# Performance work log

Measured on AMD Instinct MI355X. Metric: run time of the kernel, lower is better.

Reference implementation:

```python
import jax, jax.numpy as jnp
import numpy as np

KEY_DIM = 64
SCALE_PER_SEQ = 1.0 / np.sqrt(KEY_DIM).astype(np.float32)
SCALE_OVER_SEQS = 1.0 / np.sqrt(KEY_DIM).astype(np.float32)


def setup_inputs() -> dict:
    key = jax.random.key(0)
    ks = jax.random.split(key, 6)
    b, i, t, j, d, dv, kd = 4, 512, 32, 256, 512, 512, KEY_DIM
    w_scale = 0.05
    return {
        "input_seq": jax.random.normal(ks[0], (b, i, d), jnp.float32),
        "memory_x": jax.random.normal(ks[1], (b, t, j, d), jnp.float32),
        "memory_y": jax.random.normal(ks[2], (b, t, j, dv), jnp.float32),
        "Wq": jax.random.normal(ks[3], (d, kd), jnp.float32) * w_scale,
        "bq": jnp.zeros((kd,), jnp.float32),
        "Wk": jax.random.normal(ks[4], (d, kd), jnp.float32) * w_scale,
        "bk": jnp.zeros((kd,), jnp.float32),
        "Wv": jax.random.normal(ks[5], (dv, dv), jnp.float32) * w_scale,
        "bv": jnp.zeros((dv,), jnp.float32),
    }


def reference(input_seq, memory_x, memory_y, Wq, bq, Wk, bk, Wv, bv):
    # Projections (Dense layers)
    queries = input_seq @ Wq + bq          # [b, i, kd]
    keys = memory_x @ Wk + bk              # [b, t, j, kd]
    values = memory_y @ Wv + bv            # [b, t, j, dv]

    # Level 1: within-sequence attention
    attn_mat = jnp.einsum('bik,btjk->btij', queries, keys)          # [b, t, i, j]
    per_seq_attn = jax.nn.softmax(SCALE_PER_SEQ * attn_mat, axis=-1)
    per_seq_retrieved = jnp.einsum('btij,btjk->btik', per_seq_attn, values)  # [b, t, i, dv]

    # Level 2: over-sequences attention (max-reduce over j, softmax over t)
    mem_seq_attn = jnp.max(attn_mat, axis=-1)                       # [b, t, i]
    mem_seq_attn = jax.nn.softmax(SCALE_OVER_SEQS * mem_seq_attn, axis=1)

    retrieved = jnp.einsum('bti,btik->bik', mem_seq_attn, per_seq_retrieved)  # [b, i, dv]
    return retrieved
```

## Files before the change

### kernel.cpp

```cpp
#include <hip/hip_runtime.h>
#include <cstdint>

#define B_ 4
#define I_ 512
#define T_ 32
#define J_ 256
#define D_ 512
#define DV_ 512
#define KD_ 64
#define TJ_ (T_*J_)
#define BI_ (B_*I_)
#define MK_ (B_*T_*J_)

typedef unsigned short u16;
typedef __attribute__((ext_vector_type(8))) u16 u16x8;
typedef __attribute__((ext_vector_type(4))) u16 u16x4;
typedef __attribute__((ext_vector_type(8))) short bf16x8;
typedef __attribute__((ext_vector_type(4))) float f32x4;

__device__ __forceinline__ u16 f2bf(float f){
  unsigned u = __float_as_uint(f);
  u += 0x7fffu + ((u >> 16) & 1u);
  return (u16)(u >> 16);
}
__device__ __forceinline__ float bf2f(u16 h){ return __uint_as_float(((unsigned)h) << 16); }

#define GLD16(gsrc, ldst) __builtin_amdgcn_global_load_lds( \
    (const __attribute__((address_space(1))) unsigned int*)(gsrc), \
    (__attribute__((address_space(3))) unsigned int*)(ldst), 16, 0, 0)

__global__ __launch_bounds__(256) void k_prep(const float* __restrict__ Y, u16* __restrict__ Yt,
                                              const float* __restrict__ Wq, const float* __restrict__ Wk,
                                              const float* __restrict__ Wv, u16* __restrict__ wqt,
                                              u16* __restrict__ wkt, u16* __restrict__ wvt){
  __shared__ __align__(16) u16 tileT[64][72];
  int bid = blockIdx.x;
  int tid = threadIdx.x;
  if (bid < 4096){
    int kx = bid & 127, ny = (bid >> 7) & 7, b = bid >> 10;
    int k0 = kx*64, n0 = ny*64;
    #pragma unroll
    for (int s=0;s<4;++s){
      int idx = tid + s*256; int r = idx>>4, c4 = idx&15;
      const float4 v = *(const float4*)&Y[((size_t)b*TJ_ + k0 + r)*DV_ + n0 + c4*4];
      tileT[c4*4+0][r] = f2bf(v.x);
      tileT[c4*4+1][r] = f2bf(v.y);
      tileT[c4*4+2][r] = f2bf(v.z);
      tileT[c4*4+3][r] = f2bf(v.w);
    }
    __syncthreads();
    #pragma unroll
    for (int s=0;s<2;++s){
      int idx = tid + s*256; int rn = idx>>3, c8 = idx&7;
      *(u16x8*)&Yt[((size_t)b*DV_ + n0 + rn)*TJ_ + k0 + c8*8] = *(const u16x8*)&tileT[rn][c8*8];
    }
  } else {
    int gid = (bid - 4096)*256 + tid;
    if (gid < 32768){
      int n = gid >> 9, k = gid & 511;
      wqt[gid] = f2bf(Wq[(size_t)k*64 + n]);
    } else if (gid < 65536){
      int g = gid - 32768;
      int n = g >> 9, k = g & 511;
      wkt[g] = f2bf(Wk[(size_t)k*64 + n]);
    } else {
      int g = gid - 65536;
      int n = g >> 9, k = g & 511;
      wvt[g] = f2bf(Wv[(size_t)k*512 + n]);
    }
  }
}

__global__ __launch_bounds__(256) void k_proj(const float* __restrict__ mx, const float* __restrict__ iseq,
                                              const u16* __restrict__ wkt, const u16* __restrict__ wqt,
                                              const float* __restrict__ bk, const float* __restrict__ bq,
                                              u16* __restrict__ kbf, u16* __restrict__ qbf){
  __shared__ __align__(16) u16 As[32][72];
  __shared__ __align__(16) u16 Bs[64][72];
  int bid = blockIdx.x;
  const float* A; const u16* Bt; const float* bias; u16* C; int row0;
  if (bid < 1024){ A = mx;   Bt = wkt; bias = bk; C = kbf; row0 = bid*32; }
  else           { A = iseq; Bt = wqt; bias = bq; C = qbf; row0 = (bid-1024)*32; }
  int tid = threadIdx.x;
  int lane = tid & 63, wv = tid >> 6;
  int lrow = lane & 15, lk8 = (lane >> 4) * 8;
  int mf = wv >> 1, nfb = (wv & 1) * 2;
  int ar = tid >> 4, ac4 = tid & 15;
  int br = tid >> 3, bc8 = tid & 7;
  f32x4 acc[2];
  acc[0] = (f32x4){0.f,0.f,0.f,0.f}; acc[1] = (f32x4){0.f,0.f,0.f,0.f};

  float4 fa[2][2]; u16x8 fb[2][2];
  #define PROJ_LOAD(pp, k0) { \
    fa[pp][0] = *(const float4*)&A[(size_t)(row0 + ar)*512 + (k0) + ac4*4]; \
    fa[pp][1] = *(const float4*)&A[(size_t)(row0 + ar + 16)*512 + (k0) + ac4*4]; \
    fb[pp][0] = *(const u16x8*)&Bt[(size_t)br*512 + (k0) + bc8*8]; \
    fb[pp][1] = *(const u16x8*)&Bt[(size_t)(br+32)*512 + (k0) + bc8*8]; }

  PROJ_LOAD(0, 0)
  #pragma unroll
  for (int t=0;t<8;++t){
    const int p = t & 1;
    if (t) __syncthreads();
    if (t < 7) PROJ_LOAD(p^1, (t+1)*64)
    #pragma unroll
    for (int s=0;s<2;++s){
      u16x4 o; o[0]=f2bf(fa[p][s].x); o[1]=f2bf(fa[p][s].y); o[2]=f2bf(fa[p][s].z); o[3]=f2bf(fa[p][s].w);
      *(u16x4*)&As[ar + 16*s][ac4*4] = o;
      *(u16x8*)&Bs[br + 32*s][bc8*8] = fb[p][s];
    }
    __syncthreads();
    #pragma unroll
    for (int kk=0;kk<2;++kk){
      bf16x8 a = *(const bf16x8*)&As[mf*16 + lrow][kk*32 + lk8];
      #pragma unroll
      for (int n2=0;n2<2;++n2){
        bf16x8 bb = *(const bf16x8*)&Bs[(nfb+n2)*16 + lrow][kk*32 + lk8];
        acc[n2] = __builtin_amdgcn_mfma_f32_16x16x32_bf16(a, bb, acc[n2], 0, 0, 0);
      }
    }
  }
  #undef PROJ_LOAD
  __syncthreads();
  u16* R = &As[0][0];
  #pragma unroll
  for (int n2=0;n2<2;++n2)
    #pragma unroll
    for (int r=0;r<4;++r){
      int row = mf*16 + (lane>>4)*4 + r;
      int col = (nfb+n2)*16 + lrow;
      R[row*64 + col] = f2bf(acc[n2][r] + bias[col]);
    }
  __syncthreads();
  {
    int row = tid >> 3, c8 = tid & 7;
    *(u16x8*)&C[(size_t)(row0+row)*64 + c8*8] = *(const u16x8*)&R[row*64 + c8*8];
  }
}

__global__ __launch_bounds__(256) void k_score(const u16* __restrict__ Qbf, const u16* __restrict__ Kbf,
                                               u16* __restrict__ P, float* __restrict__ mb, float* __restrict__ zb){
  __shared__ __align__(16) u16 Qs[64][72];
  __shared__ __align__(16) u16 Ks[256][72];
  __shared__ float smax[4][64];
  __shared__ float ssum[4][64];
  __shared__ float mrow[64];
  int tid = threadIdx.x;
  int i0 = blockIdx.x*64, t = blockIdx.y, b = blockIdx.z;
  int lane = tid & 63, wv = tid >> 6;
  int lrow = lane & 15, lk = (lane >> 4) * 8;

  #pragma unroll
  for (int s=0;s<2;++s){
    int idx = tid + s*256; int r = idx>>3, c8 = idx&7;
    *(u16x8*)&Qs[r][c8*8] = *(const u16x8*)&Qbf[((size_t)b*I_ + i0 + r)*KD_ + c8*8];
  }
  #pragma unroll
  for (int s=0;s<8;++s){
    int idx = tid + s*256; int r = idx>>3, c8 = idx&7;
    *(u16x8*)&Ks[r][c8*8] = *(const u16x8*)&Kbf[(((size_t)b*T_ + t)*J_ + r)*KD_ + c8*8];
  }
  __syncthreads();

  f32x4 acc[4][4];
  #pragma unroll
  for (int i=0;i<4;++i)
    #pragma unroll
    for (int j=0;j<4;++j) acc[i][j] = (f32x4){0.f,0.f,0.f,0.f};

  #pragma unroll
  for (int kk=0;kk<2;++kk){
    bf16x8 a[4], bb[4];
    #pragma unroll
    for (int mf=0;mf<4;++mf) a[mf] = *(const bf16x8*)&Qs[mf*16 + lrow][kk*32 + lk];
    #pragma unroll
    for (int nf=0;nf<4;++nf) bb[nf] = *(const bf16x8*)&Ks[wv*64 + nf*16 + lrow][kk*32 + lk];
    #pragma unroll
    for (int mf=0;mf<4;++mf)
      #pragma unroll
      for (int nf=0;nf<4;++nf)
        acc[mf][nf] = __builtin_amdgcn_mfma_f32_16x16x32_bf16(a[mf], bb[nf], acc[mf][nf], 0, 0, 0);
  }

  #pragma unroll
  for (int mf=0;mf<4;++mf)
    #pragma unroll
    for (int r=0;r<4;++r){
      float v = acc[mf][0][r];
      #pragma unroll
      for (int nf=1;nf<4;++nf) v = fmaxf(v, acc[mf][nf][r]);
      v = fmaxf(v, __shfl_xor(v, 1));
      v = fmaxf(v, __shfl_xor(v, 2));
      v = fmaxf(v, __shfl_xor(v, 4));
      v = fmaxf(v, __shfl_xor(v, 8));
      if (lrow == 0) smax[wv][mf*16 + (lane>>4)*4 + r] = v;
    }
  __syncthreads();
  if (tid < 64){
    float m = fmaxf(fmaxf(smax[0][tid], smax[1][tid]), fmaxf(smax[2][tid], smax[3][tid]));
    mrow[tid] = m;
    mb[((size_t)b*T_ + t)*I_ + i0 + tid] = m;
  }
  __syncthreads();

  #pragma unroll
  for (int mf=0;mf<4;++mf)
    #pragma unroll
    for (int r=0;r<4;++r){
      int row = mf*16 + (lane>>4)*4 + r;
      float M = mrow[row];
      float ssm = 0.f;
      #pragma unroll
      for (int nf=0;nf<4;++nf){
        float p = __expf(0.125f*(acc[mf][nf][r] - M));
        acc[mf][nf][r] = p;
        ssm += p;
      }
      ssm += __shfl_xor(ssm, 1);
      ssm += __shfl_xor(ssm, 2);
      ssm += __shfl_xor(ssm, 4);
      ssm += __shfl_xor(ssm, 8);
      if (lrow == 0) ssum[wv][row] = ssm;
    }
  __syncthreads();
  if (tid < 64){
    float z = ssum[0][tid] + ssum[1][tid] + ssum[2][tid] + ssum[3][tid];
    zb[((size_t)b*T_ + t)*I_ + i0 + tid] = z;
  }

  u16* Ps = &Ks[0][0];
  #pragma unroll
  for (int mf=0;mf<4;++mf)
    #pragma unroll
    for (int nf=0;nf<4;++nf)
      #pragma unroll
      for (int r=0;r<4;++r){
        int row = mf*16 + (lane>>4)*4 + r;
        int col = wv*64 + nf*16 + lrow;
        Ps[row*264 + col] = f2bf(acc[mf][nf][r]);
      }
  __syncthreads();
  #pragma unroll
  for (int s=0;s<8;++s){
    int idx = tid + s*256; int r = idx>>5, c8 = idx&31;
    *(u16x8*)&P[(((size_t)b*T_ + t)*I_ + i0 + r)*J_ + c8*8] = *(const u16x8*)&Ps[r*264 + c8*8];
  }
}

template<int CH>
__global__ __launch_bounds__(256,4) void k_passB(const u16* __restrict__ P, const float* __restrict__ mbp,
                                                 const float* __restrict__ zbp, const u16* __restrict__ Yt,
                                                 u16* __restrict__ Up){
  constexpr int TPC = T_/CH;
  constexpr int NS = TPC*4;
  __shared__ __align__(16) u16 As[128*64];
  __shared__ __align__(16) u16 Bs[64*64];
  __shared__ float cs[TPC][128];
  int tid = threadIdx.x;
  int lane = tid & 63, wv = tid >> 6, wm = wv >> 1, wn = wv & 1;
  int lrow = lane & 15, lg = lane >> 4;

  int logical = (blockIdx.x & 7)*128 + (blockIdx.x >> 3);
  int group = logical >> 5, within = logical & 31;
  int ix = within & 3, ny = within >> 2;
  int b = group / CH, ch = group % CH;
  int i0 = ix*128, n0 = ny*64;

  int l8 = lane >> 3, sl = lane & 7;

  auto STAGE = [&](int step){
    int tt = step >> 2, st = step & 3;
    int t = ch*TPC + tt, j0 = st*64;
    const u16* Pbase = &P[(((size_t)b*T_ + t)*I_ + i0)*J_];
    const u16* Ybase = &Yt[((size_t)b*DV_ + n0)*TJ_ + (size_t)t*J_];
    #pragma unroll
    for (int s=0;s<4;++s){
      int row = (wv*4+s)*8 + l8;
      int colA = j0 + ((sl ^ (row & 7)) << 3);
      GLD16(Pbase + (size_t)row*J_ + colA, (u16*)As + (wv*4+s)*512);
    }
    #pragma unroll
    for (int s=0;s<2;++s){
      int row = (wv*2+s)*8 + l8;
      int colA = j0 + ((sl ^ (row & 7)) << 3);
      GLD16(Ybase + (size_t)row*TJ_ + colA, (u16*)Bs + (wv*2+s)*512);
    }
  };

  STAGE(0);

  if (tid < 128){
    int i = i0 + tid;
    float w[T_];
    float lmax = -3.0e38f;
    #pragma unroll
    for (int t=0;t<T_;++t){
      float mt = 0.125f * mbp[((size_t)b*T_ + t)*I_ + i];
      w[t] = mt;
      lmax = fmaxf(lmax, mt);
    }
    float W = 0.f;
    #pragma unroll
    for (int t=0;t<T_;++t){ float e = __expf(w[t] - lmax); w[t] = e; W += e; }
    float inv = 1.f / W;
    #pragma unroll
    for (int tt=0;tt<TPC;++tt)
      cs[tt][tid] = w[ch*TPC+tt] * inv / zbp[((size_t)b*T_ + ch*TPC + tt)*I_ + i];
  }
  __syncthreads();

  f32x4 acc[4][2];
  #pragma unroll
  for (int i=0;i<4;++i)
    #pragma unroll
    for (int j=0;j<2;++j) acc[i][j] = (f32x4){0.f,0.f,0.f,0.f};

  for (int tt = 0; tt < TPC; ++tt){
    if (tt){
      #pragma unroll
      for (int mf=0;mf<4;++mf)
        #pragma unroll
        for (int r=0;r<4;++r){
          int row = wm*64 + mf*16 + lg*4 + r;
          float ratio = cs[tt-1][row] / cs[tt][row];
          #pragma unroll
          for (int nf=0;nf<2;++nf) acc[mf][nf][r] *= ratio;
        }
    }
    #pragma unroll
    for (int st = 0; st < 4; ++st){
      const int step = tt*4 + st;
      #pragma unroll
      for (int kk=0;kk<2;++kk){
        bf16x8 a[4], bb[2];
        #pragma unroll
        for (int mf=0;mf<4;++mf){
          int ar = wm*64 + mf*16 + lrow;
          int off = ar*128 + ((kk*64 + lg*16) ^ ((ar & 7) << 4));
          a[mf] = *(const bf16x8*)((const char*)As + off);
        }
        #pragma unroll
        for (int nf=0;nf<2;++nf){
          int br = wn*32 + nf*16 + lrow;
          int off = br*128 + ((kk*64 + lg*16) ^ ((br & 7) << 4));
          bb[nf] = *(const bf16x8*)((const char*)Bs + off);
        }
        #pragma unroll
        for (int mf=0;mf<4;++mf)
          #pragma unroll
          for (int nf=0;nf<2;++nf)
            acc[mf][nf] = __builtin_amdgcn_mfma_f32_16x16x32_bf16(a[mf], bb[nf], acc[mf][nf], 0, 0, 0);
      }
      if (step + 1 < NS){
        __syncthreads();
        STAGE(step + 1);
        __syncthreads();
      }
    }
  }

  __syncthreads();
  u16* R = (u16*)&As[0];
  #pragma unroll
  for (int mf=0;mf<4;++mf)
    #pragma unroll
    for (int r=0;r<4;++r){
      int row = wm*64 + mf*16 + lg*4 + r;
      float cfin = cs[TPC-1][row];
      #pragma unroll
      for (int nf=0;nf<2;++nf){
        int col = wn*32 + nf*16 + lrow;
        R[row*64 + col] = f2bf(acc[mf][nf][r] * cfin);
      }
    }
  __syncthreads();
  u16* Ub = &Up[(size_t)ch*BI_*DV_ + ((size_t)b*I_ + i0)*DV_ + n0];
  #pragma unroll
  for (int s=0;s<4;++s){
    int id = tid + s*256;
    int row = id >> 3, c8 = id & 7;
    *(u16x8*)&Ub[(size_t)row*DV_ + c8*8] = *(const u16x8*)&R[row*64 + c8*8];
  }
}

template<int CH>
__global__ __launch_bounds__(256) void k_final(const u16* __restrict__ Up, const u16* __restrict__ Bt,
                                               const float* __restrict__ bv, float* __restrict__ out){
  __shared__ __align__(16) u16 As[32][72];
  __shared__ __align__(16) u16 Bs[64][72];
  int tid = threadIdx.x;
  int lane = tid & 63, wv = tid >> 6;
  int lrow = lane & 15, lk8 = (lane >> 4) * 8;
  int bid = blockIdx.x;
  int swz = (bid & 7)*64 + (bid >> 3);
  int row0 = (swz >> 3)*32, col0 = (swz & 7)*64;
  int mf = wv >> 1, nfb = (wv & 1)*2;
  const size_t S = (size_t)BI_*DV_;
  int ar = tid >> 3, ac8 = tid & 7;
  f32x4 acc[2];
  acc[0] = (f32x4){0.f,0.f,0.f,0.f}; acc[1] = (f32x4){0.f,0.f,0.f,0.f};

  u16x8 pa[2][CH]; u16x8 rb[2][2];
  #define FIN_LOAD(pp, k0) { \
    _Pragma("unroll") \
    for (int c=0;c<CH;++c) pa[pp][c] = *(const u16x8*)&Up[(size_t)c*S + (size_t)(row0+ar)*512 + (k0) + ac8*8]; \
    _Pragma("unroll") \
    for (int s=0;s<2;++s) rb[pp][s] = *(const u16x8*)&Bt[(size_t)(col0 + (tid>>3) + 32*s)*512 + (k0) + ac8*8]; }

  FIN_LOAD(0, 0)
  #pragma unroll
  for (int t=0;t<8;++t){
    const int p = t & 1;
    if (t) __syncthreads();
    if (t < 7) FIN_LOAD(p^1, (t+1)*64)
    u16x8 o;
    #pragma unroll
    for (int e=0;e<8;++e){
      float v = 0.f;
      #pragma unroll
      for (int c=0;c<CH;++c) v += bf2f(pa[p][c][e]);
      o[e] = f2bf(v);
    }
    *(u16x8*)&As[ar][ac8*8] = o;
    #pragma unroll
    for (int s=0;s<2;++s) *(u16x8*)&Bs[(tid>>3) + 32*s][ac8*8] = rb[p][s];
    __syncthreads();
    #pragma unroll
    for (int kk=0;kk<2;++kk){
      bf16x8 a = *(const bf16x8*)&As[mf*16 + lrow][kk*32 + lk8];
      #pragma unroll
      for (int n2=0;n2<2;++n2){
        bf16x8 bb = *(const bf16x8*)&Bs[(nfb+n2)*16 + lrow][kk*32 + lk8];
        acc[n2] = __builtin_amdgcn_mfma_f32_16x16x32_bf16(a, bb, acc[n2], 0, 0, 0);
      }
    }
  }
  #undef FIN_LOAD
  #pragma unroll
  for (int n2=0;n2<2;++n2)
    #pragma unroll
    for (int r=0;r<4;++r){
      int row = row0 + mf*16 + (lane>>4)*4 + r;
      int col = col0 + (nfb+n2)*16 + lrow;
      out[(size_t)row*DV_ + col] = acc[n2][r] + bv[col];
    }
}

extern "C" void kernel_launch(void* const* d_in, const int* in_sizes, int n_in,
                              void* d_out, int out_size, void* d_ws, size_t ws_size,
                              hipStream_t stream){
  const float* input_seq = (const float*)d_in[0];
  const float* memory_x  = (const float*)d_in[1];
  const float* memory_y  = (const float*)d_in[2];
  const float* Wq = (const float*)d_in[3];
  const float* bq = (const float*)d_in[4];
  const float* Wk = (const float*)d_in[5];
  const float* bk = (const float*)d_in[6];
  const float* Wv = (const float*)d_in[7];
  const float* bv = (const float*)d_in[8];
  float* out = (float*)d_out;

  char* ws = (char*)d_ws;
  size_t off = 0;
  auto alloc = [&](size_t bytes)->void*{
    void* p = ws + off; off += (bytes + 255) & ~(size_t)255; return p;
  };
  u16*   wqt = (u16*)  alloc((size_t)KD_*D_*2);
  u16*   wkt = (u16*)  alloc((size_t)KD_*D_*2);
  u16*   wvt = (u16*)  alloc((size_t)DV_*DV_*2);
  u16*   qbf = (u16*)  alloc((size_t)BI_*KD_*2);
  u16*   kbf = (u16*)  alloc((size_t)MK_*KD_*2);
  u16*   yt  = (u16*)  alloc((size_t)B_*DV_*TJ_*2);
  u16*   Pb  = (u16*)  alloc((size_t)B_*T_*I_*J_*2);
  float* mb  = (float*)alloc((size_t)B_*T_*I_*4);
  float* zb  = (float*)alloc((size_t)B_*T_*I_*4);
  u16*   Up  = (u16*)  alloc((size_t)8*BI_*DV_*2);

  k_prep<<<4096 + 1280, 256, 0, stream>>>(memory_y, yt, Wq, Wk, Wv, wqt, wkt, wvt);
  k_proj<<<1024 + 64, 256, 0, stream>>>(memory_x, input_seq, wkt, wqt, bk, bq, kbf, qbf);
  k_score<<<dim3(I_/64, T_, B_), 256, 0, stream>>>(qbf, kbf, Pb, mb, zb);
  k_passB<8><<<32*B_*8, 256, 0, stream>>>(Pb, mb, zb, yt, Up);
  k_final<8><<<512, 256, 0, stream>>>(Up, wvt, bv, out);
}
```

Before: 96.19 us.

## Load P operand directly to registers and double-buffer value tiles in LDS

In the pass-B GEMM, the P operand is now read straight from global memory into registers instead of being staged through LDS. The value-operand (Yt) tile is double-buffered in LDS, with the next tile's load issued before the current step's MFMAs. This drops from two barriers per k-step to one, and shrinks LDS use. The cost is that each A element is now fetched from global memory by both column waves, and those per-lane 16-byte loads are strided by a full row, so they coalesce less well than the old staged path.

```diff
diff --git a/kernel.cpp b/kernel.cpp
--- a/kernel.cpp
+++ b/kernel.cpp
@@ -253,8 +253,7 @@
                                                  u16* __restrict__ Up){
   constexpr int TPC = T_/CH;
   constexpr int NS = TPC*4;
-  __shared__ __align__(16) u16 As[128*64];
-  __shared__ __align__(16) u16 Bs[64*64];
+  __shared__ __align__(16) u16 Bs[2][64*64];
   __shared__ float cs[TPC][128];
   int tid = threadIdx.x;
   int lane = tid & 63, wv = tid >> 6, wm = wv >> 1, wn = wv & 1;
@@ -268,26 +267,19 @@
 
   int l8 = lane >> 3, sl = lane & 7;
 
-  auto STAGE = [&](int step){
+  auto STAGEB = [&](int step, int pp){
     int tt = step >> 2, st = step & 3;
     int t = ch*TPC + tt, j0 = st*64;
-    const u16* Pbase = &P[(((size_t)b*T_ + t)*I_ + i0)*J_];
     const u16* Ybase = &Yt[((size_t)b*DV_ + n0)*TJ_ + (size_t)t*J_];
-    #pragma unroll
-    for (int s=0;s<4;++s){
-      int row = (wv*4+s)*8 + l8;
-      int colA = j0 + ((sl ^ (row & 7)) << 3);
-      GLD16(Pbase + (size_t)row*J_ + colA, (u16*)As + (wv*4+s)*512);
-    }
     #pragma unroll
     for (int s=0;s<2;++s){
       int row = (wv*2+s)*8 + l8;
       int colA = j0 + ((sl ^ (row & 7)) << 3);
-      GLD16(Ybase + (size_t)row*TJ_ + colA, (u16*)Bs + (wv*2+s)*512);
+      GLD16(Ybase + (size_t)row*TJ_ + colA, (u16*)Bs[pp] + (wv*2+s)*512);
     }
   };
 
-  STAGE(0);
+  STAGEB(0, 0);
 
   if (tid < 128){
     int i = i0 + tid;
@@ -327,40 +319,40 @@
           for (int nf=0;nf<2;++nf) acc[mf][nf][r] *= ratio;
         }
     }
+    int t = ch*TPC + tt;
+    const u16* Pbase = &P[(((size_t)b*T_ + t)*I_ + i0)*J_];
     #pragma unroll
     for (int st = 0; st < 4; ++st){
       const int step = tt*4 + st;
+      const int pp = step & 1;
+      const u16* Pj = Pbase + st*64;
+      bf16x8 a[2][4];
+      #pragma unroll
+      for (int kk=0;kk<2;++kk)
+        #pragma unroll
+        for (int mf=0;mf<4;++mf)
+          a[kk][mf] = *(const bf16x8*)&Pj[(size_t)(wm*64 + mf*16 + lrow)*J_ + kk*32 + lg*8];
+      if (step + 1 < NS) STAGEB(step+1, pp^1);
       #pragma unroll
       for (int kk=0;kk<2;++kk){
-        bf16x8 a[4], bb[2];
-        #pragma unroll
-        for (int mf=0;mf<4;++mf){
-          int ar = wm*64 + mf*16 + lrow;
-          int off = ar*128 + ((kk*64 + lg*16) ^ ((ar & 7) << 4));
-          a[mf] = *(const bf16x8*)((const char*)As + off);
-        }
+        bf16x8 bb[2];
         #pragma unroll
         for (int nf=0;nf<2;++nf){
           int br = wn*32 + nf*16 + lrow;
           int off = br*128 + ((kk*64 + lg*16) ^ ((br & 7) << 4));
-          bb[nf] = *(const bf16x8*)((const char*)Bs + off);
+          bb[nf] = *(const bf16x8*)((const char*)Bs[pp] + off);
         }
         #pragma unroll
         for (int mf=0;mf<4;++mf)
           #pragma unroll
           for (int nf=0;nf<2;++nf)
-            acc[mf][nf] = __builtin_amdgcn_mfma_f32_16x16x32_bf16(a[mf], bb[nf], acc[mf][nf], 0, 0, 0);
-      }
-      if (step + 1 < NS){
-        __syncthreads();
-        STAGE(step + 1);
-        __syncthreads();
-      }
-    }
-  }
-
-  __syncthreads();
-  u16* R = (u16*)&As[0];
+            acc[mf][nf] = __builtin_amdgcn_mfma_f32_16x16x32_bf16(a[kk][mf], bb[nf], acc[mf][nf], 0, 0, 0);
+      }
+      __syncthreads();
+    }
+  }
+
+  u16* R = (u16*)&Bs[0][0];
   #pragma unroll
   for (int mf=0;mf<4;++mf)
     #pragma unroll
```

After: 135.2 us. 40.5% more time.
